# Performance work log

Measured on AMD Instinct MI355X. Metric: run time of the kernel, lower is better.

## Reference

```python
import jax, jax.numpy as jnp
import numpy as np
from jax import lax

OUT_SIZE = 224  # original input spatial size (output_size of anomaly map)
NUM_NEIGHBORS = 9
SIGMA = 4.0
KSIZE = 2 * int(4.0 * SIGMA + 0.5) + 1  # 33, kornia-style kernel size


def avg_pool3(x):
    # AvgPool2d(3, 1, 1), count_include_pad=True -> sum over 3x3 window / 9
    s = lax.reduce_window(x, 0.0, lax.add, (1, 1, 3, 3), (1, 1, 1, 1),
                          [(0, 0), (0, 0), (1, 1), (1, 1)])
    return s / 9.0


def euclidean_dist(x, y):
    # x: [..., N, E], y: [..., M, E] -> [..., N, M]
    x_norm = jnp.sum(x * x, axis=-1, keepdims=True)
    y_norm = jnp.sum(y * y, axis=-1, keepdims=True)
    res = x_norm - 2.0 * jnp.matmul(x, jnp.swapaxes(y, -2, -1)) + jnp.swapaxes(y_norm, -2, -1)
    return jnp.sqrt(jnp.clip(res, 0.0))


def gaussian_blur(x):
    # x: [B,1,H,W]; separable Gaussian, reflect padding (kornia GaussianBlur2d default)
    r = KSIZE // 2
    t = jnp.arange(KSIZE, dtype=x.dtype) - r
    k = jnp.exp(-(t * t) / (2.0 * SIGMA * SIGMA))
    k = k / jnp.sum(k)
    xp = jnp.pad(x, ((0, 0), (0, 0), (r, r), (r, r)), mode='reflect')
    kh = k.reshape(1, 1, KSIZE, 1)
    kw = k.reshape(1, 1, 1, KSIZE)
    y = lax.conv_general_dilated(xp, kh, (1, 1), 'VALID',
                                 dimension_numbers=('NCHW', 'OIHW', 'NCHW'))
    return lax.conv_general_dilated(y, kw, (1, 1), 'VALID',
                                    dimension_numbers=('NCHW', 'OIHW', 'NCHW'))


def compute_anomaly_score(patch_scores, locations, embedding, memory_bank):
    # patch_scores/locations: [B, P]; embedding: [B*P, E]; memory_bank: [M, E]
    batch, num_patches = patch_scores.shape
    bidx = jnp.arange(batch)
    max_patches = jnp.argmax(patch_scores, axis=1)                       # [B]
    max_feats = embedding.reshape(batch, num_patches, -1)[bidx, max_patches]  # [B,E]
    score = patch_scores[bidx, max_patches]                              # [B]
    nn_index = locations[bidx, max_patches]                              # [B]
    nn_sample = memory_bank[nn_index]                                    # [B,E]
    n_nb = min(NUM_NEIGHBORS, memory_bank.shape[0])
    d_bank = euclidean_dist(nn_sample, memory_bank)                      # [B,M]
    _, support = lax.top_k(-d_bank, n_nb)                                # [B,k] smallest
    sup_feats = memory_bank[support]                                     # [B,k,E]
    d = euclidean_dist(max_feats[:, None, :], sup_feats)[:, 0, :]        # [B,k]
    weights = (1.0 - jax.nn.softmax(d, axis=1))[:, 0]                    # [B]
    return weights * score


def setup_inputs() -> dict:
    key = jax.random.key(0)
    k1, k2, k3 = jax.random.split(key, 3)
    feat2 = jax.random.normal(k1, (8, 512, 28, 28), dtype=jnp.float32)
    feat3 = jax.random.normal(k2, (8, 1024, 14, 14), dtype=jnp.float32)
    memory_bank = jax.random.normal(k3, (20000, 1536), dtype=jnp.float32)
    return {'feat2': feat2, 'feat3': feat3, 'memory_bank': memory_bank}


def reference(feat2, feat3, memory_bank):
    # feature pooling (AvgPool2d(3,1,1) on each backbone layer)
    f2 = avg_pool3(feat2)
    f3 = avg_pool3(feat3)
    batch, _, height, width = f2.shape
    # generate_embedding: bilinear upsample deeper layer, concat along channels
    f3u = jax.image.resize(f3, (batch, f3.shape[1], height, width), method='bilinear')
    emb = jnp.concatenate([f2, f3u], axis=1)                 # [B,1536,28,28]
    emb_dim = emb.shape[1]
    embedding = emb.transpose(0, 2, 3, 1).reshape(-1, emb_dim)  # [B*784, 1536]
    # nearest_neighbors with n_neighbors=1
    dist = euclidean_dist(embedding, memory_bank)            # [N, M]
    patch_scores = jnp.min(dist, axis=1)
    locations = jnp.argmin(dist, axis=1)
    patch_scores = patch_scores.reshape(batch, -1)
    locations = locations.reshape(batch, -1)
    pred_score = compute_anomaly_score(patch_scores, locations, embedding, memory_bank)
    # anomaly map: bilinear upsample patch scores to input size + gaussian blur
    score_map = patch_scores.reshape(batch, 1, width, height)
    amap = jax.image.resize(score_map, (batch, 1, OUT_SIZE, OUT_SIZE), method='bilinear')
    anomaly_map = gaussian_blur(amap)
    return anomaly_map, pred_score
```

## Files before the change

### kernel.cpp

```cpp
#include <hip/hip_runtime.h>
#include <math.h>

#define NB 8
#define C2 512
#define C3 1024
#define H2 28
#define W2 28
#define H3 14
#define W3 14
#define EDIM 1536
#define PPB (H2*W2)
#define NPATCH (NB*PPB)
#define MPAD 6400
#define MBANK 20000
#define OUTW 224
#define NNB 9
#define KS 33
#define KR 16
#define NMT 25
#define NNTB 157
#define CHUNKS 8
#define CH (MBANK/CHUNKS)
#define MPB 64
#define NSLAB 24

#define SXQ 63.5f
#define SYQ (127.0f/6.0f)

typedef __attribute__((ext_vector_type(4))) int   i32x4;

#define LEXLT(va,ia,vb,ib) ((va) < (vb) || ((va)==(vb) && (ia)<(ib)))
#define CSWAP(va,ia,vb,ib) { if (LEXLT(va,ia,vb,ib)) { float _tv=(vb); int _ti=(ib); (vb)=(va); (ib)=(ia); (va)=_tv; (ia)=_ti; } }

#define BAR() asm volatile("s_barrier" ::: "memory")
#define WAITV3() asm volatile("s_waitcnt vmcnt(3)" ::: "memory")
#define WAITV0() asm volatile("s_waitcnt vmcnt(0)" ::: "memory")

__device__ __forceinline__ void gload16(const void* g, void* l) {
  __builtin_amdgcn_global_load_lds(
      (const __attribute__((address_space(1))) unsigned int*)g,
      (__attribute__((address_space(3))) unsigned int*)l, 16, 0, 0);
}
__device__ __forceinline__ signed char q8(float x, float s) {
  int v = (int)rintf(x * s);
  v = v > 127 ? 127 : (v < -127 ? -127 : v);
  return (signed char)v;
}


__global__ __launch_bounds__(256) void pool2_kernel(const float* __restrict__ in,
    float* __restrict__ emb32, signed char* __restrict__ embq) {
  int bid = blockIdx.x;
  int cg = bid & 7; int h = (bid >> 3) % H2; int b = bid / (8*H2);
  int t = threadIdx.x;
  __shared__ float s3[3][64][29];
  for (int li = t; li < 3*64*28; li += 256) {
    int w = li % 28; int c = (li/28) & 63; int dh = li/(28*64);
    int hh = h + dh - 1;
    float v = 0.f;
    if (hh >= 0 && hh < H2) v = in[((size_t)(b*C2) + cg*64 + c)*784 + hh*28 + w];
    s3[dh][c][w] = v;
  }
  __syncthreads();
  for (int o = t; o < 64*28; o += 256) {
    int c = o & 63, w = o >> 6;
    float s = 0.f;
    #pragma unroll
    for (int dh = 0; dh < 3; ++dh) {
      s += s3[dh][c][w];
      if (w > 0)  s += s3[dh][c][w-1];
      if (w < 27) s += s3[dh][c][w+1];
    }
    s *= (1.f/9.f);
    size_t idx = ((size_t)(b*PPB) + h*28 + w)*EDIM + cg*64 + c;
    emb32[idx] = s;
    embq[idx] = q8(s, SXQ);
  }
}

__global__ void pool3_kernel(const float* __restrict__ in, float* __restrict__ f3p) {
  int id = blockIdx.x*blockDim.x + threadIdx.x;
  if (id >= NB*C3*H3*W3) return;
  int w = id % W3, h = (id / W3) % H3, c = (id / (H3*W3)) % C3, b = id / (C3*H3*W3);
  const float* src = in + (size_t)(b*C3 + c)*H3*W3;
  float s = 0.f;
  #pragma unroll
  for (int dh=-1; dh<=1; ++dh) {
    int hh = h+dh; if (hh<0||hh>=H3) continue;
    #pragma unroll
    for (int dw=-1; dw<=1; ++dw) {
      int ww = w+dw; if (ww<0||ww>=W3) continue;
      s += src[hh*W3+ww];
    }
  }
  f3p[(size_t)id] = s * (1.f/9.f);
}

__global__ __launch_bounds__(256) void up3_kernel(const float* __restrict__ f3p,
    float* __restrict__ emb32, signed char* __restrict__ embq) {
  int bid = blockIdx.x;
  int cg = bid & 15; int i = (bid >> 4) % H2; int b = bid / (16*H2);
  int t = threadIdx.x;
  float sy = i*0.5f - 0.25f; sy = fminf(fmaxf(sy,0.f),(float)(H3-1));
  int y0 = (int)sy; int y1 = min(y0+1,H3-1); float fy = sy - (float)y0;
  __shared__ float r2[2][64][15];
  for (int li = t; li < 2*64*14; li += 256) {
    int w = li % 14; int c = (li/14) & 63; int yy = li/(14*64);
    int ysrc = yy ? y1 : y0;
    r2[yy][c][w] = f3p[((size_t)(b*C3) + cg*64 + c)*196 + ysrc*14 + w];
  }
  __syncthreads();
  for (int o = t; o < 64*28; o += 256) {
    int c = o & 63, j = o >> 6;
    float sx = j*0.5f - 0.25f; sx = fminf(fmaxf(sx,0.f),(float)(W3-1));
    int x0 = (int)sx; int x1 = min(x0+1,W3-1); float fx = sx - (float)x0;
    float v = (1.f-fy)*((1.f-fx)*r2[0][c][x0] + fx*r2[0][c][x1])
            +      fy *((1.f-fx)*r2[1][c][x0] + fx*r2[1][c][x1]);
    size_t idx = ((size_t)(b*PPB) + i*28 + j)*EDIM + C2 + cg*64 + c;
    emb32[idx] = v;
    embq[idx] = q8(v, SXQ);
  }
}


__global__ void bank_prep_kernel(const float* __restrict__ bank, signed char* __restrict__ bankq,
                                 float* __restrict__ yn) {
  int w = (blockIdx.x*blockDim.x + threadIdx.x) >> 6;
  int lane = threadIdx.x & 63;
  if (w >= MBANK) return;
  const float4* p = reinterpret_cast<const float4*>(bank + (size_t)w*EDIM);
  int* q = reinterpret_cast<int*>(bankq + (size_t)w*EDIM);
  float acc = 0.f;
  #pragma unroll
  for (int k = 0; k < EDIM/4/64; ++k) {
    int k4 = lane + k*64;
    float4 v = p[k4];
    acc = fmaf(v.x,v.x,acc); acc = fmaf(v.y,v.y,acc);
    acc = fmaf(v.z,v.z,acc); acc = fmaf(v.w,v.w,acc);
    unsigned pk = ((unsigned)(unsigned char)q8(v.x, SYQ))
                | ((unsigned)(unsigned char)q8(v.y, SYQ) << 8)
                | ((unsigned)(unsigned char)q8(v.z, SYQ) << 16)
                | ((unsigned)(unsigned char)q8(v.w, SYQ) << 24);
    q[k4] = (int)pk;
  }
  #pragma unroll
  for (int s = 32; s; s >>= 1) acc += __shfl_xor(acc, s);
  if (lane == 0) yn[w] = acc;
}


__global__ __launch_bounds__(512, 4) void dist_min_i8(
    const signed char* __restrict__ A, const signed char* __restrict__ B,
    const float* __restrict__ yn, float* __restrict__ outq, int* __restrict__ outi)
{
  __shared__ __align__(16) unsigned char LDSC[73728];
  const int t = threadIdx.x;
  const int lane = t & 63, wid = t >> 6;
  const int wr = wid >> 1, wc = wid & 1;

  const int nwg = NMT*NNTB;
  int orig = blockIdx.x;
  int xcd = orig & 7, loc = orig >> 3;
  int qq = nwg >> 3, rm = nwg & 7;
  int wg = (xcd < rm ? xcd*(qq+1) : rm*(qq+1) + (xcd-rm)*qq) + loc;
  const int mt = wg / NNTB, nt = wg % NNTB;
  const int m0 = mt*256, n0 = nt*128;

  const int l3 = lane >> 3, l7 = lane & 7;
  const int D = l7 ^ l3;
  const int koS = (D & 3) << 4;
  const int rhi = D >> 2;
  const int rA0 = wid*32 + (l3<<1) + rhi;
  const int rA1 = rA0 + 16;
  const int rB  = wid*16 + (l3<<1) + rhi;
  const char* Ac = (const char*)A + (size_t)m0*EDIM;
  const char* Bc = (const char*)B;
  const unsigned aoff0 = (unsigned)(rA0*EDIM + koS);
  const unsigned aoff1 = (unsigned)(rA1*EDIM + koS);
  int bn = n0 + rB; bn = bn < MBANK ? bn : MBANK-1;
  const unsigned boff = (unsigned)bn*(unsigned)EDIM + (unsigned)koS;
  char* const aDst = (char*)LDSC + wid*2048;
  char* const bDst = (char*)LDSC + 16384 + wid*1024;

  const int h = lane & 15, g = lane >> 4;
  const int csw = (((h & 1) << 2) | g) ^ (h >> 1);
  const unsigned abyte = (unsigned)(wr*4096 + (h>>1)*128 + csw*16);
  const unsigned bbyte = (unsigned)(16384 + wc*4096 + (h>>1)*128 + csw*16);

  i32x4 acc[4][4];
  #pragma unroll
  for (int i = 0; i < 4; ++i)
    #pragma unroll
    for (int j = 0; j < 4; ++j) acc[i][j] = (i32x4){0,0,0,0};

  gload16(Ac + aoff0, aDst);
  gload16(Ac + aoff1, aDst + 1024);
  gload16(Bc + boff,  bDst);
  gload16(Ac + aoff0 + 64, aDst + 24576);
  gload16(Ac + aoff1 + 64, aDst + 24576 + 1024);
  gload16(Bc + boff  + 64, bDst + 24576);
  WAITV3();
  BAR();

  #pragma unroll 3
  for (int p = 0; p < NSLAB; ++p) {
    const unsigned sb = (unsigned)(p % 3)*24576u;
    if (p < NSLAB-2) {
      const unsigned sw = (unsigned)((p+2) % 3)*24576u;
      gload16(Ac + aoff0 + (p+2)*64, aDst + sw);
      gload16(Ac + aoff1 + (p+2)*64, aDst + sw + 1024);
      gload16(Bc + boff  + (p+2)*64, bDst + sw);
    }
    i32x4 af[4], bfv[4];
    #pragma unroll
    for (int j = 0; j < 4; ++j)
      bfv[j] = *(const i32x4*)(LDSC + sb + bbyte + j*1024);
    #pragma unroll
    for (int i = 0; i < 4; ++i)
      af[i] = *(const i32x4*)(LDSC + sb + abyte + i*1024);
    __builtin_amdgcn_s_setprio(1);
    #pragma unroll
    for (int i = 0; i < 4; ++i)
      #pragma unroll
      for (int j = 0; j < 4; ++j)
        acc[i][j] = __builtin_amdgcn_mfma_i32_16x16x64_i8(af[i], bfv[j], acc[i][j], 0, 0, 0);
    __builtin_amdgcn_s_setprio(0);
    if (p < NSLAB-2) { WAITV3(); } else { WAITV0(); }
    BAR();
  }

  const float NEG2INV = -2.0f * (2.0f/127.0f) * (6.0f/127.0f);
  float ynv[4];
  #pragma unroll
  for (int j = 0; j < 4; ++j) {
    int col = n0 + wc*64 + j*16 + h;
    ynv[j] = col < MBANK ? yn[col] : INFINITY;
  }
  float* smin = (float*)LDSC;
  int* sidx = (int*)(LDSC + 2048);
  #pragma unroll
  for (int i = 0; i < 4; ++i) {
    #pragma unroll
    for (int r = 0; r < 4; ++r) {
      float v = INFINITY; int ix = 0x7fffffff;
      #pragma unroll
      for (int j = 0; j < 4; ++j) {
        float q = fmaf(NEG2INV, (float)acc[i][j][r], ynv[j]);
        int col = n0 + wc*64 + j*16 + h;
        if (q < v || (q == v && col < ix)) { v = q; ix = col; }
      }
      #pragma unroll
      for (int m = 1; m < 16; m <<= 1) {
        float ov = __shfl_xor(v, m);
        int   oi = __shfl_xor(ix, m);
        if (ov < v || (ov == v && oi < ix)) { v = ov; ix = oi; }
      }
      if (h == 0) {
        int rl = wr*64 + i*16 + g*4 + r;
        smin[rl*2 + wc] = v;
        sidx[rl*2 + wc] = ix;
      }
    }
  }
  __syncthreads();
  if (t < 256) {
    float v0 = smin[t*2], v1 = smin[t*2+1];
    int   i0 = sidx[t*2], i1 = sidx[t*2+1];
    float v; int ix;
    if (LEXLT(v1, i1, v0, i0)) { v = v1; ix = i1; } else { v = v0; ix = i0; }
    int row = m0 + t;
    if (row < NPATCH) {
      outq[(size_t)nt*NPATCH + row] = v;
      outi[(size_t)nt*NPATCH + row] = ix;
    }
  }
}


__global__ __launch_bounds__(256) void minrescore_kernel(
    const float* __restrict__ outq, const int* __restrict__ outi,
    const float* __restrict__ emb32, const float* __restrict__ bank,
    const float* __restrict__ yn, int* __restrict__ loc, float* __restrict__ ps) {
  int w = (blockIdx.x*blockDim.x + threadIdx.x) >> 6;
  int lane = threadIdx.x & 63;
  if (w >= NPATCH) return;
  float bv = INFINITY; int bi = 0x7fffffff;
  for (int s = lane; s < NNTB; s += 64) {
    float v = outq[(size_t)s*NPATCH + w];
    int  ix = outi[(size_t)s*NPATCH + w];
    if (LEXLT(v, ix, bv, bi)) { bv = v; bi = ix; }
  }
  #pragma unroll
  for (int m = 32; m; m >>= 1) {
    float ov = __shfl_xor(bv, m);
    int   oi = __shfl_xor(bi, m);
    if (LEXLT(ov, oi, bv, bi)) { bv = ov; bi = oi; }
  }
  int j = bi;
  if (lane == 0) loc[w] = j;
  const float4* x = reinterpret_cast<const float4*>(emb32 + (size_t)w*EDIM);
  const float4* y = reinterpret_cast<const float4*>(bank + (size_t)j*EDIM);
  float accd = 0.f, accx = 0.f;
  #pragma unroll
  for (int k = 0; k < EDIM/4/64; ++k) {
    float4 a = x[lane + k*64], b = y[lane + k*64];
    accd = fmaf(a.x,b.x,accd); accd = fmaf(a.y,b.y,accd);
    accd = fmaf(a.z,b.z,accd); accd = fmaf(a.w,b.w,accd);
    accx = fmaf(a.x,a.x,accx); accx = fmaf(a.y,a.y,accx);
    accx = fmaf(a.z,a.z,accx); accx = fmaf(a.w,a.w,accx);
  }
  #pragma unroll
  for (int s = 32; s; s >>= 1) { accd += __shfl_xor(accd, s); accx += __shfl_xor(accx, s); }
  if (lane == 0) ps[w] = sqrtf(fmaxf(accx - 2.f*accd + yn[j], 0.f));
}


__global__ void argmax_kernel(const float* __restrict__ ps, const int* __restrict__ loc,
                              float* __restrict__ bscore, int* __restrict__ brow, int* __restrict__ bnn) {
  __shared__ float sv[256]; __shared__ int si[256];
  int b = blockIdx.x, t = threadIdx.x;
  float bv = -INFINITY; int bi = 0x7fffffff;
  for (int p = t; p < PPB; p += 256) {
    float v = ps[b*PPB + p];
    if (v > bv || (v == bv && p < bi)) { bv = v; bi = p; }
  }
  sv[t] = bv; si[t] = bi; __syncthreads();
  for (int s = 128; s; s >>= 1) {
    if (t < s) {
      if (sv[t+s] > sv[t] || (sv[t+s] == sv[t] && si[t+s] < si[t])) { sv[t] = sv[t+s]; si[t] = si[t+s]; }
    }
    __syncthreads();
  }
  if (t == 0) {
    bscore[b] = sv[0];
    brow[b]   = b*PPB + si[0];
    bnn[b]    = loc[b*PPB + si[0]];
  }
}

__global__ __launch_bounds__(256) void dbank_kernel(
    const float* __restrict__ bank, const float* __restrict__ yn,
    const int* __restrict__ bnn, float* __restrict__ dbank)
{
  __shared__ float xs[8][EDIM];
  int t = threadIdx.x;
  for (int idx = t*4; idx < 8*EDIM; idx += 256*4) {
    int b = idx / EDIM, k = idx % EDIM;
    float4 v = *reinterpret_cast<const float4*>(bank + (size_t)bnn[b]*EDIM + k);
    *reinterpret_cast<float4*>(&xs[b][k]) = v;
  }
  __syncthreads();
  int lane = t & 63, w = t >> 6;
  for (int u = 0; u < MPB/4; ++u) {
    int m = blockIdx.x*MPB + u*4 + w;
    if (m < MBANK) {
      const float4* yp = reinterpret_cast<const float4*>(bank + (size_t)m*EDIM);
      float acc[8] = {0.f,0.f,0.f,0.f,0.f,0.f,0.f,0.f};
      for (int k4 = lane; k4 < EDIM/4; k4 += 64) {
        float4 y = yp[k4];
        int k = k4*4;
        #pragma unroll
        for (int b = 0; b < 8; ++b) {
          acc[b] = fmaf(y.x, xs[b][k+0], acc[b]);
          acc[b] = fmaf(y.y, xs[b][k+1], acc[b]);
          acc[b] = fmaf(y.z, xs[b][k+2], acc[b]);
          acc[b] = fmaf(y.w, xs[b][k+3], acc[b]);
        }
      }
      #pragma unroll
      for (int b = 0; b < 8; ++b) {
        float a = acc[b];
        #pragma unroll
        for (int s = 32; s; s >>= 1) a += __shfl_xor(a, s);
        acc[b] = a;
      }
      if (lane == 0) {
        #pragma unroll
        for (int b = 0; b < 8; ++b) {
          int nn = bnn[b];
          float d2 = yn[nn] - 2.f*acc[b] + yn[m];
          dbank[(size_t)b*MBANK + m] = sqrtf(fmaxf(d2, 0.f));
        }
      }
    }
  }
}


__global__ __launch_bounds__(256) void top9_stage1(const float* __restrict__ dbank,
                                                   float* __restrict__ cv, int* __restrict__ ci) {
  int b = blockIdx.x / CHUNKS, ch = blockIdx.x % CHUNKS;
  const float* db = dbank + (size_t)b*MBANK + ch*CH;
  int t = threadIdx.x;

  float v0=INFINITY,v1=INFINITY,v2=INFINITY,v3=INFINITY,v4=INFINITY,
        v5=INFINITY,v6=INFINITY,v7=INFINITY,v8=INFINITY;
  int i0=0x7fffffff,i1=0x7fffffff,i2=0x7fffffff,i3=0x7fffffff,i4=0x7fffffff,
      i5=0x7fffffff,i6=0x7fffffff,i7=0x7fffffff,i8=0x7fffffff;

  for (int s = 0; s < (CH+255)/256; ++s) {
    int m = t + s*256;
    if (m < CH) {
      float nv = db[m]; int ni = ch*CH + m;
      if (LEXLT(nv,ni,v8,i8)) {
        v8 = nv; i8 = ni;
        CSWAP(v8,i8,v7,i7); CSWAP(v7,i7,v6,i6); CSWAP(v6,i6,v5,i5); CSWAP(v5,i5,v4,i4);
        CSWAP(v4,i4,v3,i3); CSWAP(v3,i3,v2,i2); CSWAP(v2,i2,v1,i1); CSWAP(v1,i1,v0,i0);
      }
    }
  }

  __shared__ float sv[256*9];
  __shared__ int   si[256*9];
  __shared__ float rv[256]; __shared__ int ri[256]; __shared__ int rp[256];
  sv[t*9+0]=v0; sv[t*9+1]=v1; sv[t*9+2]=v2; sv[t*9+3]=v3; sv[t*9+4]=v4;
  sv[t*9+5]=v5; sv[t*9+6]=v6; sv[t*9+7]=v7; sv[t*9+8]=v8;
  si[t*9+0]=i0; si[t*9+1]=i1; si[t*9+2]=i2; si[t*9+3]=i3; si[t*9+4]=i4;
  si[t*9+5]=i5; si[t*9+6]=i6; si[t*9+7]=i7; si[t*9+8]=i8;
  __syncthreads();

  for (int r = 0; r < NNB; ++r) {
    float bv = INFINITY; int bix = 0x7fffffff; int bp = -1;
    #pragma unroll
    for (int u = 0; u < 9; ++u) {
      float v = sv[t*9+u]; int ix = si[t*9+u];
      if (LEXLT(v,ix,bv,bix)) { bv = v; bix = ix; bp = t*9+u; }
    }
    rv[t] = bv; ri[t] = bix; rp[t] = bp; __syncthreads();
    for (int s = 128; s; s >>= 1) {
      if (t < s) {
        if (LEXLT(rv[t+s],ri[t+s],rv[t],ri[t])) { rv[t]=rv[t+s]; ri[t]=ri[t+s]; rp[t]=rp[t+s]; }
      }
      __syncthreads();
    }
    if (t == 0) {
      cv[blockIdx.x*NNB + r] = rv[0];
      ci[blockIdx.x*NNB + r] = ri[0];
      sv[rp[0]] = INFINITY; si[rp[0]] = 0x7fffffff;
    }
    __syncthreads();
  }
}


__global__ __launch_bounds__(128) void finalize_kernel(
    const float* __restrict__ cv, const int* __restrict__ ci,
    const float* __restrict__ emb32, const float* __restrict__ bank,
    const float* __restrict__ yn, const int* __restrict__ brow,
    const float* __restrict__ bscore, float* __restrict__ out) {
  __shared__ float sv[128]; __shared__ int si[128];
  __shared__ float wv[128]; __shared__ int wi[128]; __shared__ int wp[128];
  __shared__ int supp[NNB]; __shared__ float ds[NNB];
  int b = blockIdx.x, t = threadIdx.x;
  if (t < CHUNKS*NNB) { sv[t] = cv[b*CHUNKS*NNB + t]; si[t] = ci[b*CHUNKS*NNB + t]; }
  else { sv[t] = INFINITY; si[t] = 0x7fffffff; }
  __syncthreads();
  for (int r = 0; r < NNB; ++r) {
    wv[t] = sv[t]; wi[t] = si[t]; wp[t] = t; __syncthreads();
    for (int s = 64; s; s >>= 1) {
      if (t < s) {
        if (LEXLT(wv[t+s],wi[t+s],wv[t],wi[t])) { wv[t]=wv[t+s]; wi[t]=wi[t+s]; wp[t]=wp[t+s]; }
      }
      __syncthreads();
    }
    if (t == 0) {
      supp[r] = wi[0];
      sv[wp[0]] = INFINITY; si[wp[0]] = 0x7fffffff;
    }
    __syncthreads();
  }
  int lane = t & 63, w = t >> 6;
  int row = brow[b];
  const float* x = emb32 + (size_t)row*EDIM;
  for (int j = w; j < NNB; j += 2) {
    const float* y = bank + (size_t)supp[j]*EDIM;
    float accd = 0.f, accx = 0.f;
    for (int k = lane; k < EDIM; k += 64) {
      float a = x[k];
      accd = fmaf(a, y[k], accd);
      accx = fmaf(a, a, accx);
    }
    #pragma unroll
    for (int s = 32; s; s >>= 1) { accd += __shfl_xor(accd, s); accx += __shfl_xor(accx, s); }
    if (lane == 0) ds[j] = sqrtf(fmaxf(accx - 2.f*accd + yn[supp[j]], 0.f));
  }
  __syncthreads();
  if (t == 0) {
    float mx = -INFINITY;
    #pragma unroll
    for (int j = 0; j < NNB; ++j) mx = fmaxf(mx, ds[j]);
    float s = 0.f;
    #pragma unroll
    for (int j = 0; j < NNB; ++j) s += expf(ds[j] - mx);
    float wgt = 1.f - expf(ds[0] - mx) / s;
    out[b] = wgt * bscore[b];
  }
}


__device__ __forceinline__ int refl224(int x) {
  if (x < 0) return -x;
  if (x > OUTW-1) return 2*(OUTW-1) - x;
  return x;
}

__global__ __launch_bounds__(256) void upblurh_kernel(const float* __restrict__ ps,
                                                      float* __restrict__ tmp) {
  int b = blockIdx.x / OUTW, i = blockIdx.x % OUTW;
  int t = threadIdx.x;
  __shared__ float l[W2];
  __shared__ float graw[KS];
  if (t < KS) {
    float x = (float)t - (float)KR;
    graw[t] = expf(-(x*x) / (2.f*4.f*4.f));
  }
  float sy = ((float)i + 0.5f)*0.125f - 0.5f; sy = fminf(fmaxf(sy,0.f),(float)(H2-1));
  int y0 = (int)sy; int y1 = min(y0+1,H2-1); float fy = sy - (float)y0;
  if (t < W2) {
    const float* p = ps + b*PPB;
    l[t] = (1.f-fy)*p[y0*W2+t] + fy*p[y1*W2+t];
  }
  __syncthreads();
  if (t >= OUTW) return;
  float gsum = 0.f;
  #pragma unroll
  for (int u = 0; u < KS; ++u) gsum += graw[u];
  float winv = 1.f / gsum;
  float s = 0.f;
  #pragma unroll
  for (int v = 0; v < KS; ++v) {
    int jj = refl224(t - KR + v);
    float sx = ((float)jj + 0.5f)*0.125f - 0.5f; sx = fminf(fmaxf(sx,0.f),(float)(W2-1));
    int x0 = (int)sx; int x1 = min(x0+1,W2-1); float fx = sx - (float)x0;
    s = fmaf(graw[v]*winv, (1.f-fx)*l[x0] + fx*l[x1], s);
  }
  tmp[((size_t)b*OUTW + i)*OUTW + t] = s;
}

__global__ __launch_bounds__(256) void blurv_kernel(const float* __restrict__ in,
                                                    float* __restrict__ out) {
  __shared__ float graw[KS];
  int t = threadIdx.x;
  if (t < KS) {
    float x = (float)t - (float)KR;
    graw[t] = expf(-(x*x) / (2.f*4.f*4.f));
  }
  __syncthreads();
  int id = blockIdx.x*blockDim.x + t;
  if (id >= NB*OUTW*OUTW) return;
  float gsum = 0.f;
  #pragma unroll
  for (int u = 0; u < KS; ++u) gsum += graw[u];
  float winv = 1.f / gsum;
  int j = id % OUTW, i = (id/OUTW) % OUTW, b = id/(OUTW*OUTW);
  float s = 0.f;
  #pragma unroll
  for (int u = 0; u < KS; ++u) {
    int ii = refl224(i - KR + u);
    s = fmaf(graw[u]*winv, in[((size_t)b*OUTW + ii)*OUTW + j], s);
  }
  out[id] = s;
}


extern "C" void kernel_launch(void* const* d_in, const int* in_sizes, int n_in,
                              void* d_out, int out_size, void* d_ws, size_t ws_size,
                              hipStream_t stream) {
  const float* feat2 = (const float*)d_in[0];
  const float* feat3 = (const float*)d_in[1];
  const float* bank  = (const float*)d_in[2];
  float* out = (float*)d_out;

  char* base = (char*)d_ws;
  size_t off = 0;
  auto alloc = [&](size_t nbytes) -> char* {
    char* p = base + off;
    off += ((nbytes + 255) & ~(size_t)255);
    return p;
  };
  float*       emb32 = (float*)      alloc((size_t)NPATCH*EDIM*4);
  signed char* embq  = (signed char*)alloc((size_t)MPAD*EDIM);
  signed char* bankq = (signed char*)alloc((size_t)MBANK*EDIM);
  float* f3p    = (float*)alloc((size_t)NB*C3*H3*W3*4);
  float* yn     = (float*)alloc(MBANK*4);
  float* outq   = (float*)alloc((size_t)NNTB*NPATCH*4);
  int*   outi   = (int*)  alloc((size_t)NNTB*NPATCH*4);
  float* ps     = (float*)alloc(NPATCH*4);
  int*   loc    = (int*)  alloc(NPATCH*4);
  float* bscore = (float*)alloc(NB*4);
  int*   brow   = (int*)  alloc(NB*4);
  int*   bnn    = (int*)  alloc(NB*4);
  float* dbank  = (float*)alloc((size_t)NB*MBANK*4);
  float* cv     = (float*)alloc(NB*CHUNKS*NNB*4);
  int*   ci     = (int*)  alloc(NB*CHUNKS*NNB*4);
  float* tmp    = (float*)alloc((size_t)NB*OUTW*OUTW*4);

  pool2_kernel<<<NB*H2*8, 256, 0, stream>>>(feat2, emb32, embq);
  {
    int n = NB*C3*H3*W3;
    pool3_kernel<<<(n+255)/256, 256, 0, stream>>>(feat3, f3p);
  }
  up3_kernel<<<NB*H2*16, 256, 0, stream>>>(f3p, emb32, embq);
  bank_prep_kernel<<<(MBANK*64)/256, 256, 0, stream>>>(bank, bankq, yn);

  dist_min_i8<<<NMT*NNTB, 512, 0, stream>>>(embq, bankq, yn, outq, outi);
  minrescore_kernel<<<(NPATCH*64)/256, 256, 0, stream>>>(outq, outi, emb32, bank, yn, loc, ps);

  argmax_kernel<<<NB, 256, 0, stream>>>(ps, loc, bscore, brow, bnn);
  dbank_kernel<<<(MBANK+MPB-1)/MPB, 256, 0, stream>>>(bank, yn, bnn, dbank);
  top9_stage1<<<NB*CHUNKS, 256, 0, stream>>>(dbank, cv, ci);
  finalize_kernel<<<NB, 128, 0, stream>>>(cv, ci, emb32, bank, yn, brow, bscore,
                                          out + NB*OUTW*OUTW);

  {
    upblurh_kernel<<<NB*OUTW, 256, 0, stream>>>(ps, tmp);
    int n = NB*OUTW*OUTW;
    blurv_kernel<<<(n+255)/256, 256, 0, stream>>>(tmp, out);
  }
}
```

Before: 505.6 us.

## Load B operand directly from global into registers, dropping LDS staging

The int8 distance GEMM kernel stops staging the memory-bank (B) tiles through LDS. Each wave now reads its B fragments straight from global memory into registers every slab, while only the A tiles keep the triple-buffered LDS DMA path. This shrinks LDS per block from 72 KB to 48 KB, which could allow more resident blocks. The cost is that the four wave-rows fetch the same B data redundantly, and the B load latency is exposed right before the MFMAs. The explicit vmcnt waits inside the loop were also removed, so ordering of the A prefetch against the barrier now depends on the compiler.

```diff
diff --git a/kernel.cpp b/kernel.cpp
--- a/kernel.cpp
+++ b/kernel.cpp
@@ -33,8 +33,7 @@
 #define CSWAP(va,ia,vb,ib) { if (LEXLT(va,ia,vb,ib)) { float _tv=(vb); int _ti=(ib); (vb)=(va); (ib)=(ia); (va)=_tv; (ia)=_ti; } }
 
 #define BAR() asm volatile("s_barrier" ::: "memory")
-#define WAITV3() asm volatile("s_waitcnt vmcnt(3)" ::: "memory")
-#define WAITV0() asm volatile("s_waitcnt vmcnt(0)" ::: "memory")
+#define WAITV2() asm volatile("s_waitcnt vmcnt(2)" ::: "memory")
 
 __device__ __forceinline__ void gload16(const void* g, void* l) {
   __builtin_amdgcn_global_load_lds(
@@ -153,7 +152,7 @@
     const signed char* __restrict__ A, const signed char* __restrict__ B,
     const float* __restrict__ yn, float* __restrict__ outq, int* __restrict__ outi)
 {
-  __shared__ __align__(16) unsigned char LDSC[73728];
+  __shared__ __align__(16) unsigned char LDSC[49152];
   const int t = threadIdx.x;
   const int lane = t & 63, wid = t >> 6;
   const int wr = wid >> 1, wc = wid & 1;
@@ -172,20 +171,22 @@
   const int rhi = D >> 2;
   const int rA0 = wid*32 + (l3<<1) + rhi;
   const int rA1 = rA0 + 16;
-  const int rB  = wid*16 + (l3<<1) + rhi;
   const char* Ac = (const char*)A + (size_t)m0*EDIM;
-  const char* Bc = (const char*)B;
   const unsigned aoff0 = (unsigned)(rA0*EDIM + koS);
   const unsigned aoff1 = (unsigned)(rA1*EDIM + koS);
-  int bn = n0 + rB; bn = bn < MBANK ? bn : MBANK-1;
-  const unsigned boff = (unsigned)bn*(unsigned)EDIM + (unsigned)koS;
   char* const aDst = (char*)LDSC + wid*2048;
-  char* const bDst = (char*)LDSC + 16384 + wid*1024;
 
   const int h = lane & 15, g = lane >> 4;
   const int csw = (((h & 1) << 2) | g) ^ (h >> 1);
   const unsigned abyte = (unsigned)(wr*4096 + (h>>1)*128 + csw*16);
-  const unsigned bbyte = (unsigned)(16384 + wc*4096 + (h>>1)*128 + csw*16);
+
+  const signed char* bp[4];
+  #pragma unroll
+  for (int j = 0; j < 4; ++j) {
+    int row = n0 + wc*64 + j*16 + h;
+    row = row < MBANK ? row : MBANK-1;
+    bp[j] = B + (size_t)row*EDIM + g*16;
+  }
 
   i32x4 acc[4][4];
   #pragma unroll
@@ -195,26 +196,23 @@
 
   gload16(Ac + aoff0, aDst);
   gload16(Ac + aoff1, aDst + 1024);
-  gload16(Bc + boff,  bDst);
-  gload16(Ac + aoff0 + 64, aDst + 24576);
-  gload16(Ac + aoff1 + 64, aDst + 24576 + 1024);
-  gload16(Bc + boff  + 64, bDst + 24576);
-  WAITV3();
+  gload16(Ac + aoff0 + 64, aDst + 16384);
+  gload16(Ac + aoff1 + 64, aDst + 16384 + 1024);
+  WAITV2();
   BAR();
 
-  #pragma unroll 3
   for (int p = 0; p < NSLAB; ++p) {
-    const unsigned sb = (unsigned)(p % 3)*24576u;
+    const unsigned sb = (unsigned)(p % 3) * 16384u;
+    i32x4 bfv[4];
+    #pragma unroll
+    for (int j = 0; j < 4; ++j)
+      bfv[j] = *(const i32x4*)(bp[j] + p*64);
     if (p < NSLAB-2) {
-      const unsigned sw = (unsigned)((p+2) % 3)*24576u;
+      const unsigned sw = (unsigned)((p+2) % 3) * 16384u;
       gload16(Ac + aoff0 + (p+2)*64, aDst + sw);
       gload16(Ac + aoff1 + (p+2)*64, aDst + sw + 1024);
-      gload16(Bc + boff  + (p+2)*64, bDst + sw);
-    }
-    i32x4 af[4], bfv[4];
-    #pragma unroll
-    for (int j = 0; j < 4; ++j)
-      bfv[j] = *(const i32x4*)(LDSC + sb + bbyte + j*1024);
+    }
+    i32x4 af[4];
     #pragma unroll
     for (int i = 0; i < 4; ++i)
       af[i] = *(const i32x4*)(LDSC + sb + abyte + i*1024);
@@ -225,7 +223,6 @@
       for (int j = 0; j < 4; ++j)
         acc[i][j] = __builtin_amdgcn_mfma_i32_16x16x64_i8(af[i], bfv[j], acc[i][j], 0, 0, 0);
     __builtin_amdgcn_s_setprio(0);
-    if (p < NSLAB-2) { WAITV3(); } else { WAITV0(); }
     BAR();
   }
 
```

Result: slower. 690.7 us (+36.6%).
